# Kernel optimization log

Measured on AMD Instinct MI355X. Metric: run time of the kernel, lower is better.

The kernel has to match this reference:

```python
import jax, jax.numpy as jnp
import numpy as np


def setup_inputs() -> dict:
    N, E, F, M, D = 50000, 200000, 64, 64, 128
    L = 3
    LAMBS = jnp.array([1.0, 0.1, 0.01], jnp.float32) * 12.0  # lambs * output
    R = int(np.ceil(np.sqrt(N)))  # n_virtuals = 224
    RAW = M * L + F  # raw_message_dimension = 256
    key = jax.random.key(0)
    ks = jax.random.split(key, 16)

    def lin(k, i, o):
        return jax.random.normal(k, (i, o), jnp.float32) / np.float32(np.sqrt(i))

    return dict(
        source_nodes=jax.random.randint(ks[0], (E,), 0, N),
        target_nodes=jax.random.randint(ks[1], (E,), 0, N),
        timestamps=jax.random.uniform(ks[2], (E,), jnp.float32),
        now_time=jnp.ones((1,), jnp.float32),
        predict_IND=0,
        node_features=0.1 * jax.random.normal(ks[3], (N, F), jnp.float32),
        memory=jnp.concatenate([0.05 * jax.random.normal(ks[4], (N, L, M), jnp.float32), jnp.ones((N, L, 1), jnp.float32)], axis=-1),
        last_update=jnp.zeros((N,), jnp.float32),
        virtual_memory=0.05 * jax.random.normal(ks[5], (R, L, M), jnp.float32),
        virtual_last_update=jnp.zeros((R,), jnp.float32),
        A_r=jnp.ones((N, R), jnp.float32) + jax.random.uniform(ks[6], (N, R), jnp.float32) / 10.0,
        static_emb=0.1 * jax.random.normal(ks[7], (N, D), jnp.float32),
        lamb=jnp.array([0.5], jnp.float32),
        lambs=LAMBS,
        mf_W1=lin(ks[8], RAW, RAW // 2), mf_b1=jnp.zeros((RAW // 2,), jnp.float32),
        mf_W2=lin(ks[9], RAW // 2, M), mf_b2=jnp.zeros((M,), jnp.float32),
        ffr_W1=lin(ks[10], RAW, RAW), ffr_b1=jnp.zeros((RAW,), jnp.float32),
        ffr_W2=lin(ks[11], RAW, M), ffr_b2=jnp.zeros((M,), jnp.float32),
        et_W=lin(ks[12], L * M, M), et_b=jnp.zeros((M,), jnp.float32),
        st_W=lin(ks[13], 2 * M, D), st_b=jnp.zeros((D,), jnp.float32),
    )


def reference(source_nodes, target_nodes, timestamps, now_time, predict_IND,
              node_features, memory, last_update, virtual_memory, virtual_last_update,
              A_r, static_emb, lamb, lambs,
              mf_W1, mf_b1, mf_W2, mf_b2, ffr_W1, ffr_b1, ffr_W2, ffr_b2,
              et_W, et_b, st_W, st_b):
    N, L, Mp1 = memory.shape
    M = Mp1 - 1
    R = virtual_memory.shape[0]
    E = source_nodes.shape[0]
    eps = 1e-6

    # exp_lambs embedding of targets: memory ratio [E, L*M]
    mem_t = memory[target_nodes]
    tgt_emb = (mem_t[:, :, :-1] / mem_t[:, :, -1:]).reshape(E, L * M)
    # raw message = [target_embedding, node_features[target], 1]  -> [E, RAW+1]
    src_msg = jnp.concatenate([tgt_emb, node_features[target_nodes], jnp.ones((E, 1), tgt_emb.dtype)], axis=1)

    # exp_lambs aggregation: decay every event to the latest timestamp of its source node
    t_max = jax.ops.segment_max(timestamps, source_nodes, num_segments=N)
    cnt = jax.ops.segment_sum(jnp.ones((E,), timestamps.dtype), source_nodes, num_segments=N)
    has_msg = cnt > 0
    t_max = jnp.where(has_msg, t_max, 0.0)
    w = jnp.exp(-lambs[None, :] * (t_max[source_nodes][:, None] - timestamps[:, None]))  # [E, L]
    agg = jax.ops.segment_sum(w[:, :, None] * src_msg[:, None, :], source_nodes, num_segments=N)  # [N, L, RAW+1]

    # MLP message function on feature channels, carry the weight-count channel along
    feat = agg[:, :, :-1]  # [N, L, RAW]
    h = jax.nn.relu(feat @ mf_W1 + mf_b1)
    msg_feat = jax.nn.relu(h @ mf_W2 + mf_b2)  # [N, L, M]
    messages = jnp.concatenate([msg_feat, agg[:, :, -1:]], axis=-1)  # [N, L, M+1]

    # virtual-node routing: A = softmax(A_r, axis=0) restricted to active nodes
    A = jax.nn.softmax(A_r, axis=0) * has_msg[:, None].astype(A_r.dtype)  # [N, R]
    B = jnp.where(has_msg[:, None, None], feat / jnp.maximum(agg[:, :, -1:], eps), 0.0)  # [N, L, RAW]
    vmid = jnp.einsum('nr,nlf->rlf', A, B)  # [R, L, RAW]
    vh = jax.nn.leaky_relu(vmid @ ffr_W1 + ffr_b1)
    vmsg = jax.nn.leaky_relu(vh @ ffr_W2 + ffr_b2)  # [R, L, M]

    # node memory exp-decay update (only active nodes)
    dt = jnp.where(has_msg, t_max - last_update, 0.0)
    decay = jnp.exp(-lambs[None, :, None] * dt[:, None, None])  # [N, L, 1]
    new_mem = jnp.where(has_msg[:, None, None], memory * decay + messages, memory)
    node_emb = (new_mem[:, :, :-1] / jnp.maximum(new_mem[:, :, -1:], eps)).reshape(N, L * M)

    # virtual memory exp-decay update to now_time
    vdt = now_time[0] - virtual_last_update  # [R]
    vdecay = jnp.exp(-lambs[None, :] * vdt[:, None])  # [R, L]
    new_vmem = virtual_memory * vdecay[:, :, None] + vmsg
    v_emb = new_vmem.reshape(R, L * M)

    r2n = jax.nn.softmax(A_r, axis=1)  # [N, R]
    vnode_emb = r2n @ v_emb  # [N, L*M]

    dyn = jnp.concatenate([node_emb, vnode_emb], axis=0)  # [2N, L*M]
    hh = jax.nn.leaky_relu(dyn @ et_W + et_b)  # [2N, M]
    hh = hh.reshape(2, N, M).transpose(1, 0, 2).reshape(N, 2 * M)
    spat = jax.nn.leaky_relu(hh @ st_W + st_b)  # [N, D]
    return lamb[0] * static_emb + (1.0 - lamb[0]) * spat
```

## Files before the change

### kernel.cpp

```cpp
#include <hip/hip_runtime.h>

static __device__ __forceinline__ float lky(float x) { return x > 0.f ? x : 0.01f * x; }

static __device__ __forceinline__ unsigned short f2bf(float x) {
    unsigned int u = __float_as_uint(x);
    unsigned int r = (u + 0x7FFFu + ((u >> 16) & 1u)) >> 16;
    return (unsigned short)r;
}
static __device__ __forceinline__ float bf2f(unsigned short x) {
    return __uint_as_float((unsigned int)x << 16);
}
static __device__ __forceinline__ unsigned int pack2bf(float lo, float hi) {
    return (unsigned int)f2bf(lo) | ((unsigned int)f2bf(hi) << 16);
}

typedef __attribute__((ext_vector_type(8))) short short8;
typedef __attribute__((ext_vector_type(4))) float f32x4;

constexpr int SN  = 50048;
constexpr int KLV = 608;
constexpr int VCM = 83;
constexpr int NSCAN = 53248;

__global__ void k_init(float* t_max, int* cnt, int* cursor, float* colsum, int N, int NP) {
    int i = blockIdx.x * 256 + threadIdx.x;
    if (i < N) { t_max[i] = -1.0f; cursor[i] = 0; }
    if (i < NP) cnt[i] = 0;
    if (i < 224) colsum[i] = 0.0f;
}

__global__ void k_tbf(const float* __restrict__ src, unsigned short* __restrict__ dst,
                      int K, int C) {
    int i = blockIdx.x * 256 + threadIdx.x;
    if (i >= K * C) return;
    int c = i / K, k = i % K;
    dst[i] = f2bf(src[k * C + c]);
}

__global__ void k_tmax_cnt(const int* __restrict__ src, const float* __restrict__ ts,
                           float* t_max, int* cnt, int E) {
    int e = blockIdx.x * 256 + threadIdx.x;
    if (e >= E) return;
    int s = src[e];
    atomicMax((int*)(t_max + s), __float_as_int(ts[e]));
    atomicAdd(cnt + s, 1);
}

__global__ __launch_bounds__(1024) void k_scan(const int* __restrict__ cnt,
                                               int* __restrict__ offsets, int N) {
    __shared__ int wsum[16];
    __shared__ int s_run;
    int t = threadIdx.x;
    int lane = t & 63, wid = t >> 6;
    if (t == 0) s_run = 0;
    __syncthreads();
    int nchunk = (N + 4095) >> 12;
    for (int c = 0; c < nchunk; ++c) {
        int i0 = (c << 12) + t * 4;
        int4 v = *(const int4*)(cnt + i0);
        int s = v.x + v.y + v.z + v.w;
        int x = s;
        #pragma unroll
        for (int d = 1; d < 64; d <<= 1) {
            int y = __shfl_up(x, d, 64);
            if (lane >= d) x += y;
        }
        if (lane == 63) wsum[wid] = x;
        __syncthreads();
        int wbase = 0;
        #pragma unroll
        for (int w = 0; w < 16; ++w) wbase += (w < wid) ? wsum[w] : 0;
        int run = s_run;
        int base = run + wbase + x - s;
        if (i0 + 3 < N) {
            int4 o;
            o.x = base; o.y = base + v.x; o.z = o.y + v.y; o.w = o.z + v.z;
            *(int4*)(offsets + i0) = o;
        } else {
            int o = base;
            if (i0 < N) offsets[i0] = o;
            o += v.x;
            if (i0 + 1 < N) offsets[i0 + 1] = o;
            o += v.y;
            if (i0 + 2 < N) offsets[i0 + 2] = o;
            o += v.z;
            if (i0 + 3 < N) offsets[i0 + 3] = o;
        }
        __syncthreads();
        if (t == 1023) s_run = run + wbase + x;
        __syncthreads();
    }
    if (t == 0) offsets[N] = s_run;
}

__global__ void k_scatter(const int* __restrict__ src, const int* __restrict__ offsets,
                          int* cursor, int* sorted, int E) {
    int e = blockIdx.x * 256 + threadIdx.x;
    if (e >= E) return;
    int s = src[e];
    int pos = offsets[s] + atomicAdd(cursor + s, 1);
    sorted[pos] = e;
}

__global__ __launch_bounds__(256) void k_prep(
        const float* __restrict__ memory, const float* __restrict__ nodef,
        unsigned int* __restrict__ temb, int N) {
    int wid = threadIdx.x >> 6, lane = threadIdx.x & 63;
    int n = blockIdx.x * 4 + wid;
    if (n >= N) return;
    const float* mrow = memory + (size_t)n * 195;
    float d0 = mrow[64], d1 = mrow[129], d2 = mrow[194];
    int f = 2 * lane;
    float den = (f < 64) ? d0 : d1;
    int offA = (f < 64) ? f : f + 1;
    float va0 = mrow[offA] / den;
    float va1 = mrow[offA + 1] / den;
    float vb0, vb1;
    if (lane < 32) {
        vb0 = mrow[130 + 2 * lane] / d2;
        vb1 = mrow[131 + 2 * lane] / d2;
    } else {
        const float* nf = nodef + (size_t)n * 64 + 2 * (lane - 32);
        vb0 = nf[0]; vb1 = nf[1];
    }
    temb[(size_t)n * 128 + lane]      = pack2bf(va0, va1);
    temb[(size_t)n * 128 + 64 + lane] = pack2bf(vb0, vb1);
}

__global__ __launch_bounds__(256) void k_aexp(
        const float* __restrict__ A_r,
        float* __restrict__ rowsum, float* __restrict__ colsum,
        unsigned short* __restrict__ AexpT, unsigned short* __restrict__ Aexp_rm, int N) {
    __shared__ unsigned short sE[64][228];
    int t = threadIdx.x;
    int n0 = blockIdx.x * 64;
    int maxq = min(64, N - n0) * 56;
    const float4* src = (const float4*)(A_r + (size_t)n0 * 224);
    #pragma unroll
    for (int k = 0; k < 14; ++k) {
        int i = t + k * 256;
        float4 v = (i < maxq) ? src[i] : (float4){-1e30f, -1e30f, -1e30f, -1e30f};
        int row = i / 56, cq = i % 56;
        uint2 pk;
        pk.x = pack2bf(__expf(v.x), __expf(v.y));
        pk.y = pack2bf(__expf(v.z), __expf(v.w));
        *(uint2*)&sE[row][cq * 4] = pk;
    }
    __syncthreads();
    {
        int row = t >> 2, q = t & 3;
        const uint2* p = (const uint2*)&sE[row][q * 56];
        float s = 0.f;
        #pragma unroll
        for (int c = 0; c < 7; ++c) {
            uint2 u = p[c];
            s += __uint_as_float(u.x << 16) + __uint_as_float(u.x & 0xffff0000u)
               + __uint_as_float(u.y << 16) + __uint_as_float(u.y & 0xffff0000u);
        }
        s += __shfl_xor(s, 1, 64);
        s += __shfl_xor(s, 2, 64);
        if (q == 0 && n0 + row < N) rowsum[n0 + row] = s;
    }
    if (t < 224) {
        float s = 0.f;
        #pragma unroll 8
        for (int r = 0; r < 64; ++r) s += bf2f(sE[r][t]);
        atomicAdd(colsum + t, s);
    }
    {
        unsigned int* dst = (unsigned int*)Aexp_rm;
        for (int i = t; i < 64 * 112; i += 256) {
            int n = i / 112, cp = i % 112;
            dst[(size_t)(n0 + n) * 112 + cp] = *(const unsigned int*)&sE[n][2 * cp];
        }
    }
    {
        unsigned int* dst = (unsigned int*)AexpT;
        for (int u = t; u < 224 * 32; u += 256) {
            int r = u >> 5, np = u & 31;
            unsigned int lo = sE[2 * np][r];
            unsigned int hi = sE[2 * np + 1][r];
            dst[(size_t)r * (SN / 2) + (n0 >> 1) + np] = lo | (hi << 16);
        }
    }
}

__global__ __launch_bounds__(256) void k_agg(
        const int* __restrict__ tgt, const float* __restrict__ ts,
        const int* __restrict__ sorted, const int* __restrict__ offsets,
        const float* __restrict__ t_max, const unsigned int* __restrict__ temb,
        const float* __restrict__ lambs,
        unsigned int* __restrict__ aggb, float* __restrict__ cnt3,
        int* __restrict__ has_msg, int N) {
    int wid = threadIdx.x >> 6, lane = threadIdx.x & 63;
    int n = blockIdx.x * 4 + wid;
    size_t rb = (size_t)n * 3;
    if (n >= N) {
        #pragma unroll
        for (int l = 0; l < 3; ++l) {
            unsigned int* row = aggb + (rb + l) * 128;
            row[lane] = 0; row[64 + lane] = 0;
            if (lane == 0) cnt3[rb + l] = 0.f;
        }
        return;
    }
    int beg = offsets[n], end = offsets[n + 1];
    float lb0 = lambs[0], lb1 = lambs[1], lb2 = lambs[2];
    float tm = t_max[n];
    float aa0[3], aa1[3], ab0[3], ab1[3], accc[3];
    #pragma unroll
    for (int l = 0; l < 3; ++l) { aa0[l] = aa1[l] = ab0[l] = ab1[l] = accc[l] = 0.f; }
    for (int idx = beg; idx < end; ++idx) {
        int e = sorted[idx];
        int tt = tgt[e];
        float d = tm - ts[e];
        unsigned int ua = temb[(size_t)tt * 128 + lane];
        unsigned int ub = temb[(size_t)tt * 128 + 64 + lane];
        float a0 = __uint_as_float(ua << 16);
        float a1 = __uint_as_float(ua & 0xffff0000u);
        float b0 = __uint_as_float(ub << 16);
        float b1 = __uint_as_float(ub & 0xffff0000u);
        float w0 = __expf(-lb0 * d), w1 = __expf(-lb1 * d), w2 = __expf(-lb2 * d);
        aa0[0] += w0 * a0; aa1[0] += w0 * a1; ab0[0] += w0 * b0; ab1[0] += w0 * b1; accc[0] += w0;
        aa0[1] += w1 * a0; aa1[1] += w1 * a1; ab0[1] += w1 * b0; ab1[1] += w1 * b1; accc[1] += w1;
        aa0[2] += w2 * a0; aa1[2] += w2 * a1; ab0[2] += w2 * b0; ab1[2] += w2 * b1; accc[2] += w2;
    }
    #pragma unroll
    for (int l = 0; l < 3; ++l) {
        unsigned int* row = aggb + (rb + l) * 128;
        row[lane]      = pack2bf(aa0[l], aa1[l]);
        row[64 + lane] = pack2bf(ab0[l], ab1[l]);
        if (lane == 0) cnt3[rb + l] = accc[l];
    }
    if (lane == 0) has_msg[n] = (end > beg) ? 1 : 0;
}

__global__ __launch_bounds__(256) void k_mf_mfma(
        const unsigned short* __restrict__ aggb,
        const unsigned short* __restrict__ W1T, const float* __restrict__ b1,
        const unsigned short* __restrict__ W2T, const float* __restrict__ b2,
        unsigned short* __restrict__ msg_feat, int NROWS) {
    __shared__ unsigned short As[64 * 264];
    __shared__ unsigned short Hs[64 * 136];
    int t = threadIdx.x, lane = t & 63, w = t >> 6;
    int lr = lane & 15, kg = lane >> 4;
    int row0 = blockIdx.x * 64;
    {
        int r = t >> 2, s4 = t & 3;
        const uint4* src = (const uint4*)(aggb + (size_t)(row0 + r) * 256 + s4 * 64);
        uint4* dst = (uint4*)(As + r * 264 + s4 * 64);
        #pragma unroll
        for (int u = 0; u < 8; ++u) dst[u] = src[u];
    }
    __syncthreads();
    int n0 = w * 32;
    f32x4 acc[4][2];
    #pragma unroll
    for (int m = 0; m < 4; ++m) {
        acc[m][0] = (f32x4){0.f, 0.f, 0.f, 0.f};
        acc[m][1] = (f32x4){0.f, 0.f, 0.f, 0.f};
    }
    for (int kk = 0; kk < 8; ++kk) {
        short8 bf0 = *(const short8*)(W1T + (size_t)(n0 + lr) * 256 + kk * 32 + kg * 8);
        short8 bf1 = *(const short8*)(W1T + (size_t)(n0 + 16 + lr) * 256 + kk * 32 + kg * 8);
        #pragma unroll
        for (int m = 0; m < 4; ++m) {
            short8 af = *(const short8*)(As + (m * 16 + lr) * 264 + kk * 32 + kg * 8);
            acc[m][0] = __builtin_amdgcn_mfma_f32_16x16x32_bf16(af, bf0, acc[m][0], 0, 0, 0);
            acc[m][1] = __builtin_amdgcn_mfma_f32_16x16x32_bf16(af, bf1, acc[m][1], 0, 0, 0);
        }
    }
    float bb0 = b1[n0 + lr], bb1 = b1[n0 + 16 + lr];
    #pragma unroll
    for (int m = 0; m < 4; ++m)
        #pragma unroll
        for (int j = 0; j < 4; ++j) {
            int row = m * 16 + kg * 4 + j;
            Hs[row * 136 + n0 + lr]      = f2bf(fmaxf(acc[m][0][j] + bb0, 0.f));
            Hs[row * 136 + n0 + 16 + lr] = f2bf(fmaxf(acc[m][1][j] + bb1, 0.f));
        }
    __syncthreads();
    int c0 = w * 16;
    f32x4 a2[4];
    #pragma unroll
    for (int m = 0; m < 4; ++m) a2[m] = (f32x4){0.f, 0.f, 0.f, 0.f};
    for (int kk = 0; kk < 4; ++kk) {
        short8 bf = *(const short8*)(W2T + (size_t)(c0 + lr) * 128 + kk * 32 + kg * 8);
        #pragma unroll
        for (int m = 0; m < 4; ++m) {
            short8 af = *(const short8*)(Hs + (m * 16 + lr) * 136 + kk * 32 + kg * 8);
            a2[m] = __builtin_amdgcn_mfma_f32_16x16x32_bf16(af, bf, a2[m], 0, 0, 0);
        }
    }
    float b2v = b2[c0 + lr];
    #pragma unroll
    for (int m = 0; m < 4; ++m)
        #pragma unroll
        for (int j = 0; j < 4; ++j) {
            int row = row0 + m * 16 + kg * 4 + j;
            if (row < NROWS)
                msg_feat[(size_t)row * 64 + c0 + lr] = f2bf(fmaxf(a2[m][j] + b2v, 0.f));
        }
}

__global__ __launch_bounds__(256) void k_vmid_mfma(
        const unsigned short* __restrict__ AexpT, const unsigned short* __restrict__ aggb,
        const float* __restrict__ cnt3, float* __restrict__ vpart) {
    __shared__ unsigned short As[112 * 40];
    __shared__ unsigned int BsT[128 * 20];
    int bx = blockIdx.x;
    int chunk = bx / 12, tile = bx % 12;
    int r0 = (tile & 1) * 112;
    int ft = tile >> 1;
    int l = ft >> 1, fo = (ft & 1) * 128;
    int t = threadIdx.x, lane = t & 63, w = t >> 6;
    int lr = lane & 15, kg = lane >> 4;
    int np = t >> 4, sg = t & 15;
    f32x4 acc[7][2];
    #pragma unroll
    for (int q = 0; q < 7; ++q) {
        acc[q][0] = (f32x4){0.f, 0.f, 0.f, 0.f};
        acc[q][1] = (f32x4){0.f, 0.f, 0.f, 0.f};
    }
    int nbeg = chunk * KLV;
    int nsteps = min(KLV, SN - nbeg) >> 5;
    int c0 = w * 32 + lr, c1 = c0 + 16;
    int rb0 = c0 * 20 + (kg ^ ((c0 >> 3) & 3)) * 4;
    int rb1 = c1 * 20 + (kg ^ ((c1 >> 3) & 3)) * 4;
    int swz = np ^ ((sg & 3) << 2);
    for (int s = 0; s < nsteps; ++s) {
        int n0 = nbeg + s * 32;
        if (t < 224) {
            int srow = t >> 1, sseg = t & 1;
            const uint4* ap = (const uint4*)(AexpT + (size_t)(r0 + srow) * SN + n0) + sseg * 2;
            uint4 v0 = ap[0];
            uint4 v1 = ap[1];
            *(uint4*)&As[srow * 40 + sseg * 16]     = v0;
            *(uint4*)&As[srow * 40 + sseg * 16 + 8] = v1;
        }
        {
            int na = n0 + 2 * np;
            size_t ra = ((size_t)na * 3 + l) * 256 + fo + sg * 8;
            uint4 va = *(const uint4*)(aggb + ra);
            uint4 vb = *(const uint4*)(aggb + ra + 768);
            float da = 1.f / fmaxf(cnt3[(size_t)na * 3 + l], 1e-6f);
            float db = 1.f / fmaxf(cnt3[(size_t)na * 3 + l + 3], 1e-6f);
            const unsigned short* pa = (const unsigned short*)&va;
            const unsigned short* pb = (const unsigned short*)&vb;
            unsigned int* dst = BsT + sg * 160 + swz;
            #pragma unroll
            for (int j = 0; j < 8; ++j)
                dst[j * 20] = pack2bf(bf2f(pa[j]) * da, bf2f(pb[j]) * db);
        }
        __syncthreads();
        short8 b0 = *(const short8*)((const unsigned short*)(BsT + rb0));
        short8 b1 = *(const short8*)((const unsigned short*)(BsT + rb1));
        #pragma unroll
        for (int q = 0; q < 7; ++q) {
            short8 af = *(const short8*)&As[(q * 16 + lr) * 40 + kg * 8];
            acc[q][0] = __builtin_amdgcn_mfma_f32_16x16x32_bf16(af, b0, acc[q][0], 0, 0, 0);
            acc[q][1] = __builtin_amdgcn_mfma_f32_16x16x32_bf16(af, b1, acc[q][1], 0, 0, 0);
        }
        __syncthreads();
    }
    float* outp = vpart + (size_t)chunk * 172032;
    #pragma unroll
    for (int q = 0; q < 7; ++q) {
        int row = r0 + q * 16 + kg * 4;
        #pragma unroll
        for (int p = 0; p < 2; ++p) {
            int col = l * 256 + fo + w * 32 + p * 16 + lr;
            #pragma unroll
            for (int j = 0; j < 4; ++j)
                outp[(size_t)(row + j) * 768 + col] = acc[q][p][j];
        }
    }
}

__global__ void k_vred(const float* __restrict__ vpart, const float* __restrict__ colsum,
                       float* __restrict__ vmid) {
    int idx = blockIdx.x * 256 + threadIdx.x;
    if (idx >= 224 * 768) return;
    float s = 0.f;
    for (int c = 0; c < VCM; ++c) s += vpart[(long)c * (224 * 768) + idx];
    vmid[idx] = s / colsum[idx / 768];
}

__global__ __launch_bounds__(256) void k_ffr(
        const float* __restrict__ vmid, const float* __restrict__ W1, const float* __restrict__ b1,
        const float* __restrict__ W2, const float* __restrict__ b2,
        const float* __restrict__ vmem, const float* __restrict__ vlast,
        const float* __restrict__ lambs, const float* __restrict__ now_time,
        unsigned short* __restrict__ vembT) {
    __shared__ float sin_[16][260];
    __shared__ float svh[16][260];
    int row0 = blockIdx.x * 16;
    int t = threadIdx.x;
    #pragma unroll
    for (int k = 0; k < 16; ++k) {
        int idx = t + k * 256;
        int r = idx >> 8, f = idx & 255;
        sin_[r][f] = vmid[(long)(row0 + r) * 256 + f];
    }
    __syncthreads();
    {
        int cg = t & 63, rg = t >> 6;
        int c0 = cg * 4, r0 = rg * 4;
        float acc[4][4];
        #pragma unroll
        for (int i = 0; i < 4; ++i)
            #pragma unroll
            for (int j = 0; j < 4; ++j) acc[i][j] = 0.f;
        for (int f0 = 0; f0 < 256; f0 += 4) {
            float4 a[4];
            #pragma unroll
            for (int i = 0; i < 4; ++i) a[i] = *(const float4*)&sin_[r0 + i][f0];
            #pragma unroll
            for (int ff = 0; ff < 4; ++ff) {
                float4 w = *(const float4*)&W1[(long)(f0 + ff) * 256 + c0];
                #pragma unroll
                for (int i = 0; i < 4; ++i) {
                    float av = (&a[i].x)[ff];
                    acc[i][0] += av * w.x; acc[i][1] += av * w.y;
                    acc[i][2] += av * w.z; acc[i][3] += av * w.w;
                }
            }
        }
        #pragma unroll
        for (int i = 0; i < 4; ++i)
            #pragma unroll
            for (int j = 0; j < 4; ++j)
                svh[r0 + i][c0 + j] = lky(acc[i][j] + b1[c0 + j]);
    }
    __syncthreads();
    {
        int cg = t & 31, rg = t >> 5;
        int c0 = cg * 2, r0 = rg * 2;
        float acc[2][2];
        acc[0][0] = acc[0][1] = acc[1][0] = acc[1][1] = 0.f;
        for (int f0 = 0; f0 < 256; f0 += 4) {
            float4 a[2];
            #pragma unroll
            for (int i = 0; i < 2; ++i) a[i] = *(const float4*)&svh[r0 + i][f0];
            #pragma unroll
            for (int ff = 0; ff < 4; ++ff) {
                float2 w = *(const float2*)&W2[(long)(f0 + ff) * 64 + c0];
                #pragma unroll
                for (int i = 0; i < 2; ++i) {
                    float av = (&a[i].x)[ff];
                    acc[i][0] += av * w.x; acc[i][1] += av * w.y;
                }
            }
        }
        float nowv = now_time[0];
        #pragma unroll
        for (int i = 0; i < 2; ++i) {
            int row = row0 + r0 + i;
            int rr = row / 3, l = row % 3;
            float vd = __expf(-lambs[l] * (nowv - vlast[rr]));
            #pragma unroll
            for (int j = 0; j < 2; ++j) {
                float v = lky(acc[i][j] + b2[c0 + j]);
                int m = c0 + j;
                vembT[(size_t)(l * 64 + m) * 224 + rr] =
                    f2bf(vmem[(long)rr * 192 + l * 64 + m] * vd + v);
            }
        }
    }
}

__global__ void k_newmem(const float* __restrict__ memory,
        const unsigned short* __restrict__ msg_feat,
        const float* __restrict__ cnt3, const float* __restrict__ t_max,
        const float* __restrict__ last_update, const int* __restrict__ has_msg,
        const float* __restrict__ lambs, unsigned short* __restrict__ node_emb, int N) {
    int n = blockIdx.x;
    int j = threadIdx.x;
    int l = j >> 6, m = j & 63;
    int has = has_msg[n];
    float dt = has ? (t_max[n] - last_update[n]) : 0.f;
    float decay = __expf(-lambs[l] * dt);
    long mb = (long)n * 195 + l * 65;
    float num = memory[mb + m];
    float den = memory[mb + 64];
    if (has) {
        num = num * decay + bf2f(msg_feat[(size_t)n * 192 + j]);
        den = den * decay + cnt3[(size_t)n * 3 + l];
    }
    node_emb[(size_t)n * 192 + j] = f2bf(num / fmaxf(den, 1e-6f));
}

__global__ __launch_bounds__(256) void k_vnode_mfma(
        const unsigned short* __restrict__ Aexp_rm, const unsigned short* __restrict__ vembT,
        const float* __restrict__ rowsum, unsigned short* __restrict__ vnode_emb, int N) {
    __shared__ unsigned short As[64 * 232];
    __shared__ float sRS[64];
    int t = threadIdx.x, lane = t & 63, w = t >> 6;
    int lr = lane & 15, kg = lane >> 4;
    int row0 = blockIdx.x * 64;
    {
        int r = t >> 2, sg = t & 3;
        const uint4* src = (const uint4*)(Aexp_rm + (size_t)(row0 + r) * 224 + sg * 56);
        uint4* dst = (uint4*)(As + r * 232 + sg * 56);
        #pragma unroll
        for (int u = 0; u < 7; ++u) dst[u] = src[u];
    }
    if (t < 64) sRS[t] = rowsum[min(row0 + t, N - 1)];
    __syncthreads();
    int n0 = w * 48;
    f32x4 acc[4][3];
    #pragma unroll
    for (int m = 0; m < 4; ++m)
        #pragma unroll
        for (int nt = 0; nt < 3; ++nt) acc[m][nt] = (f32x4){0.f, 0.f, 0.f, 0.f};
    for (int kk = 0; kk < 7; ++kk) {
        short8 bf[3];
        #pragma unroll
        for (int nt = 0; nt < 3; ++nt)
            bf[nt] = *(const short8*)(vembT + (size_t)(n0 + nt * 16 + lr) * 224 + kk * 32 + kg * 8);
        #pragma unroll
        for (int m = 0; m < 4; ++m) {
            short8 af = *(const short8*)(As + (m * 16 + lr) * 232 + kk * 32 + kg * 8);
            #pragma unroll
            for (int nt = 0; nt < 3; ++nt)
                acc[m][nt] = __builtin_amdgcn_mfma_f32_16x16x32_bf16(af, bf[nt], acc[m][nt], 0, 0, 0);
        }
    }
    #pragma unroll
    for (int m = 0; m < 4; ++m)
        #pragma unroll
        for (int j = 0; j < 4; ++j) {
            int row = row0 + m * 16 + kg * 4 + j;
            if (row < N) {
                float inv = 1.f / sRS[row - row0];
                #pragma unroll
                for (int nt = 0; nt < 3; ++nt)
                    vnode_emb[(size_t)row * 192 + n0 + nt * 16 + lr] = f2bf(acc[m][nt][j] * inv);
            }
        }
}

__global__ __launch_bounds__(256) void k_et_st_mfma(
        const unsigned short* __restrict__ ne, const unsigned short* __restrict__ ve,
        const unsigned short* __restrict__ etWT, const float* __restrict__ etb,
        const unsigned short* __restrict__ stWT, const float* __restrict__ stb,
        const float* __restrict__ stat, const float* __restrict__ lamb,
        float* __restrict__ out, int N) {
    __shared__ unsigned short As[128 * 200];
    __shared__ unsigned short Hs[64 * 136];
    int t = threadIdx.x, lane = t & 63, w = t >> 6;
    int lr = lane & 15, kg = lane >> 4;
    int row0 = blockIdx.x * 64;
    {
        int r = t >> 2, sg = t & 3;
        const uint4* sn = (const uint4*)(ne + (size_t)(row0 + r) * 192 + sg * 48);
        const uint4* sv = (const uint4*)(ve + (size_t)(row0 + r) * 192 + sg * 48);
        uint4* dn = (uint4*)(As + (size_t)r * 200 + sg * 48);
        uint4* dv = (uint4*)(As + (size_t)(64 + r) * 200 + sg * 48);
        #pragma unroll
        for (int u = 0; u < 6; ++u) { dn[u] = sn[u]; dv[u] = sv[u]; }
    }
    __syncthreads();
    int c0 = w * 16;
    f32x4 acc[2][4];
    #pragma unroll
    for (int h = 0; h < 2; ++h)
        #pragma unroll
        for (int m = 0; m < 4; ++m) acc[h][m] = (f32x4){0.f, 0.f, 0.f, 0.f};
    for (int kk = 0; kk < 6; ++kk) {
        short8 bf = *(const short8*)(etWT + (size_t)(c0 + lr) * 192 + kk * 32 + kg * 8);
        #pragma unroll
        for (int h = 0; h < 2; ++h)
            #pragma unroll
            for (int m = 0; m < 4; ++m) {
                short8 af = *(const short8*)(As + (size_t)(h * 64 + m * 16 + lr) * 200 + kk * 32 + kg * 8);
                acc[h][m] = __builtin_amdgcn_mfma_f32_16x16x32_bf16(af, bf, acc[h][m], 0, 0, 0);
            }
    }
    float bb = etb[c0 + lr];
    #pragma unroll
    for (int h = 0; h < 2; ++h)
        #pragma unroll
        for (int m = 0; m < 4; ++m)
            #pragma unroll
            for (int j = 0; j < 4; ++j)
                Hs[(m * 16 + kg * 4 + j) * 136 + h * 64 + c0 + lr] = f2bf(lky(acc[h][m][j] + bb));
    __syncthreads();
    int c0s = w * 32;
    f32x4 a2[4][2];
    #pragma unroll
    for (int m = 0; m < 4; ++m) { a2[m][0] = (f32x4){0.f,0.f,0.f,0.f}; a2[m][1] = (f32x4){0.f,0.f,0.f,0.f}; }
    for (int kk = 0; kk < 4; ++kk) {
        short8 bf0 = *(const short8*)(stWT + (size_t)(c0s + lr) * 128 + kk * 32 + kg * 8);
        short8 bf1 = *(const short8*)(stWT + (size_t)(c0s + 16 + lr) * 128 + kk * 32 + kg * 8);
        #pragma unroll
        for (int m = 0; m < 4; ++m) {
            short8 af = *(const short8*)(Hs + (m * 16 + lr) * 136 + kk * 32 + kg * 8);
            a2[m][0] = __builtin_amdgcn_mfma_f32_16x16x32_bf16(af, bf0, a2[m][0], 0, 0, 0);
            a2[m][1] = __builtin_amdgcn_mfma_f32_16x16x32_bf16(af, bf1, a2[m][1], 0, 0, 0);
        }
    }
    float lam = lamb[0];
    float sb0 = stb[c0s + lr], sb1 = stb[c0s + 16 + lr];
    #pragma unroll
    for (int m = 0; m < 4; ++m)
        #pragma unroll
        for (int j = 0; j < 4; ++j) {
            int n = row0 + m * 16 + kg * 4 + j;
            if (n < N) {
                int ca = c0s + lr, cb = c0s + 16 + lr;
                float va = lky(a2[m][0][j] + sb0);
                float vb = lky(a2[m][1][j] + sb1);
                out[(size_t)n * 128 + ca] = lam * stat[(size_t)n * 128 + ca] + (1.f - lam) * va;
                out[(size_t)n * 128 + cb] = lam * stat[(size_t)n * 128 + cb] + (1.f - lam) * vb;
            }
        }
}

extern "C" void kernel_launch(void* const* d_in, const int* in_sizes, int n_in,
                              void* d_out, int out_size, void* d_ws, size_t ws_size,
                              hipStream_t stream) {
    const int*   src        = (const int*)d_in[0];
    const int*   tgt        = (const int*)d_in[1];
    const float* ts         = (const float*)d_in[2];
    const float* now_time   = (const float*)d_in[3];
    const float* nodef      = (const float*)d_in[5];
    const float* memory     = (const float*)d_in[6];
    const float* last_upd   = (const float*)d_in[7];
    const float* vmem       = (const float*)d_in[8];
    const float* vlast      = (const float*)d_in[9];
    const float* A_r        = (const float*)d_in[10];
    const float* static_emb = (const float*)d_in[11];
    const float* lamb       = (const float*)d_in[12];
    const float* lambs      = (const float*)d_in[13];
    const float* mf_W1      = (const float*)d_in[14];
    const float* mf_b1      = (const float*)d_in[15];
    const float* mf_W2      = (const float*)d_in[16];
    const float* mf_b2      = (const float*)d_in[17];
    const float* ffr_W1     = (const float*)d_in[18];
    const float* ffr_b1     = (const float*)d_in[19];
    const float* ffr_W2     = (const float*)d_in[20];
    const float* ffr_b2     = (const float*)d_in[21];
    const float* et_W       = (const float*)d_in[22];
    const float* et_b       = (const float*)d_in[23];
    const float* st_W       = (const float*)d_in[24];
    const float* st_b       = (const float*)d_in[25];

    int E = in_sizes[0];
    int N = in_sizes[7];

    float* ws = (float*)d_ws;
    size_t off = 0;
    auto alloc = [&](size_t nf) { float* p = ws + off; off += (nf + 63) & ~(size_t)63; return p; };
    unsigned short* aggb  = (unsigned short*)alloc((size_t)SN * 384);
    unsigned short* msg_feat = (unsigned short*)alloc((size_t)N * 96);
    unsigned short* AexpT   = (unsigned short*)alloc((size_t)224 * SN / 2);
    unsigned short* Aexp_rm = (unsigned short*)alloc((size_t)SN * 224 / 2);
    float* tv_union = alloc((size_t)VCM * 172032);
    float* vmid     = alloc(224 * 768);
    unsigned short* vembT = (unsigned short*)alloc((size_t)192 * 224 / 2 + 64);
    float* t_max    = alloc(N);
    float* rowsum   = alloc(N);
    float* cnt3     = alloc((size_t)SN * 3);
    float* colsum   = alloc(256);
    unsigned short* W1T  = (unsigned short*)alloc(128 * 256 / 2);
    unsigned short* W2T  = (unsigned short*)alloc(64 * 128 / 2);
    unsigned short* etWT = (unsigned short*)alloc(64 * 192 / 2);
    unsigned short* stWT = (unsigned short*)alloc(128 * 128 / 2);
    int*   cnt      = (int*)alloc(NSCAN);
    int*   offsets  = (int*)alloc(N + 1);
    int*   cursor   = (int*)alloc(N);
    int*   sorted   = (int*)alloc(E);
    int*   has_msg  = (int*)alloc(N);
    if (off * sizeof(float) > ws_size) return;

    unsigned int* temb = (unsigned int*)tv_union;
    float* vpart = tv_union;
    unsigned short* node_emb  = (unsigned short*)aggb;
    unsigned short* vnode_emb = node_emb + (size_t)N * 192;

    k_init<<<(NSCAN + 255) / 256, 256, 0, stream>>>(t_max, cnt, cursor, colsum, N, NSCAN);
    k_tbf<<<(256 * 128 + 255) / 256, 256, 0, stream>>>(mf_W1, W1T, 256, 128);
    k_tbf<<<(128 * 64 + 255) / 256, 256, 0, stream>>>(mf_W2, W2T, 128, 64);
    k_tbf<<<(192 * 64 + 255) / 256, 256, 0, stream>>>(et_W, etWT, 192, 64);
    k_tbf<<<(128 * 128 + 255) / 256, 256, 0, stream>>>(st_W, stWT, 128, 128);
    k_tmax_cnt<<<(E + 255) / 256, 256, 0, stream>>>(src, ts, t_max, cnt, E);
    k_scan<<<1, 1024, 0, stream>>>(cnt, offsets, N);
    k_scatter<<<(E + 255) / 256, 256, 0, stream>>>(src, offsets, cursor, sorted, E);
    k_prep<<<(N + 3) / 4, 256, 0, stream>>>(memory, nodef, temb, N);
    k_aexp<<<SN / 64, 256, 0, stream>>>(A_r, rowsum, colsum, AexpT, Aexp_rm, N);
    k_agg<<<SN / 4, 256, 0, stream>>>(tgt, ts, sorted, offsets, t_max, temb,
                                      lambs, (unsigned int*)aggb, cnt3, has_msg, N);
    k_mf_mfma<<<SN * 3 / 64, 256, 0, stream>>>(aggb, W1T, mf_b1, W2T, mf_b2, msg_feat, N * 3);
    k_vmid_mfma<<<12 * VCM, 256, 0, stream>>>(AexpT, aggb, cnt3, vpart);
    k_vred<<<(224 * 768 + 255) / 256, 256, 0, stream>>>(vpart, colsum, vmid);
    k_ffr<<<42, 256, 0, stream>>>(vmid, ffr_W1, ffr_b1, ffr_W2, ffr_b2, vmem, vlast,
                                  lambs, now_time, vembT);
    k_newmem<<<N, 192, 0, stream>>>(memory, msg_feat, cnt3, t_max, last_upd, has_msg,
                                    lambs, node_emb, N);
    k_vnode_mfma<<<SN / 64, 256, 0, stream>>>(Aexp_rm, vembT, rowsum, vnode_emb, N);
    k_et_st_mfma<<<SN / 64, 256, 0, stream>>>(node_emb, vnode_emb, etWT, et_b, stWT, st_b,
                                              static_emb, lamb, (float*)d_out, N);
}
```

Before: 385.0 us.

## Read MFMA A-operands directly from global and remap vmid blocks per XCD

Three MFMA kernels (mf, vnode, et_st) no longer stage their A tiles in shared memory. Each wave now loads its A fragments straight from global memory, which removes the LDS copy and a barrier and lowers LDS use so more blocks can be resident. The cost is that every wave re-reads the same A rows from global/L2 instead of sharing one LDS copy. Separately, the vmid kernel remaps block IDs so that consecutive virtual blocks, which share chunks of the A and aggregate data, land on the same XCD for better L2 locality.

```diff
diff --git a/kernel.cpp b/kernel.cpp
--- a/kernel.cpp
+++ b/kernel.cpp
@@ -21,6 +21,9 @@
 constexpr int KLV = 608;
 constexpr int VCM = 83;
 constexpr int NSCAN = 53248;
+constexpr int NWG_V = 12 * VCM;
+constexpr int NQ_V  = NWG_V / 8;
+constexpr int NR_V  = NWG_V % 8;
 
 __global__ void k_init(float* t_max, int* cnt, int* cursor, float* colsum, int N, int NP) {
     int i = blockIdx.x * 256 + threadIdx.x;
@@ -240,19 +243,11 @@
         const unsigned short* __restrict__ W1T, const float* __restrict__ b1,
         const unsigned short* __restrict__ W2T, const float* __restrict__ b2,
         unsigned short* __restrict__ msg_feat, int NROWS) {
-    __shared__ unsigned short As[64 * 264];
     __shared__ unsigned short Hs[64 * 136];
     int t = threadIdx.x, lane = t & 63, w = t >> 6;
     int lr = lane & 15, kg = lane >> 4;
     int row0 = blockIdx.x * 64;
-    {
-        int r = t >> 2, s4 = t & 3;
-        const uint4* src = (const uint4*)(aggb + (size_t)(row0 + r) * 256 + s4 * 64);
-        uint4* dst = (uint4*)(As + r * 264 + s4 * 64);
-        #pragma unroll
-        for (int u = 0; u < 8; ++u) dst[u] = src[u];
-    }
-    __syncthreads();
+    const unsigned short* abase = aggb + (size_t)row0 * 256;
     int n0 = w * 32;
     f32x4 acc[4][2];
     #pragma unroll
@@ -265,7 +260,7 @@
         short8 bf1 = *(const short8*)(W1T + (size_t)(n0 + 16 + lr) * 256 + kk * 32 + kg * 8);
         #pragma unroll
         for (int m = 0; m < 4; ++m) {
-            short8 af = *(const short8*)(As + (m * 16 + lr) * 264 + kk * 32 + kg * 8);
+            short8 af = *(const short8*)(abase + (size_t)(m * 16 + lr) * 256 + kk * 32 + kg * 8);
             acc[m][0] = __builtin_amdgcn_mfma_f32_16x16x32_bf16(af, bf0, acc[m][0], 0, 0, 0);
             acc[m][1] = __builtin_amdgcn_mfma_f32_16x16x32_bf16(af, bf1, acc[m][1], 0, 0, 0);
         }
@@ -309,7 +304,10 @@
     __shared__ unsigned short As[112 * 40];
     __shared__ unsigned int BsT[128 * 20];
     int bx = blockIdx.x;
-    int chunk = bx / 12, tile = bx % 12;
+    int xcd = bx & 7, bidx = bx >> 3;
+    int virt = (xcd < NR_V) ? xcd * (NQ_V + 1) + bidx
+                            : NR_V * (NQ_V + 1) + (xcd - NR_V) * NQ_V + bidx;
+    int chunk = virt / 12, tile = virt % 12;
     int r0 = (tile & 1) * 112;
     int ft = tile >> 1;
     int l = ft >> 1, fo = (ft & 1) * 128;
@@ -493,18 +491,11 @@
 __global__ __launch_bounds__(256) void k_vnode_mfma(
         const unsigned short* __restrict__ Aexp_rm, const unsigned short* __restrict__ vembT,
         const float* __restrict__ rowsum, unsigned short* __restrict__ vnode_emb, int N) {
-    __shared__ unsigned short As[64 * 232];
     __shared__ float sRS[64];
     int t = threadIdx.x, lane = t & 63, w = t >> 6;
     int lr = lane & 15, kg = lane >> 4;
     int row0 = blockIdx.x * 64;
-    {
-        int r = t >> 2, sg = t & 3;
-        const uint4* src = (const uint4*)(Aexp_rm + (size_t)(row0 + r) * 224 + sg * 56);
-        uint4* dst = (uint4*)(As + r * 232 + sg * 56);
-        #pragma unroll
-        for (int u = 0; u < 7; ++u) dst[u] = src[u];
-    }
+    const unsigned short* abase = Aexp_rm + (size_t)row0 * 224;
     if (t < 64) sRS[t] = rowsum[min(row0 + t, N - 1)];
     __syncthreads();
     int n0 = w * 48;
@@ -520,7 +511,7 @@
             bf[nt] = *(const short8*)(vembT + (size_t)(n0 + nt * 16 + lr) * 224 + kk * 32 + kg * 8);
         #pragma unroll
         for (int m = 0; m < 4; ++m) {
-            short8 af = *(const short8*)(As + (m * 16 + lr) * 232 + kk * 32 + kg * 8);
+            short8 af = *(const short8*)(abase + (size_t)(m * 16 + lr) * 224 + kk * 32 + kg * 8);
             #pragma unroll
             for (int nt = 0; nt < 3; ++nt)
                 acc[m][nt] = __builtin_amdgcn_mfma_f32_16x16x32_bf16(af, bf[nt], acc[m][nt], 0, 0, 0);
@@ -546,21 +537,10 @@
         const unsigned short* __restrict__ stWT, const float* __restrict__ stb,
         const float* __restrict__ stat, const float* __restrict__ lamb,
         float* __restrict__ out, int N) {
-    __shared__ unsigned short As[128 * 200];
     __shared__ unsigned short Hs[64 * 136];
     int t = threadIdx.x, lane = t & 63, w = t >> 6;
     int lr = lane & 15, kg = lane >> 4;
     int row0 = blockIdx.x * 64;
-    {
-        int r = t >> 2, sg = t & 3;
-        const uint4* sn = (const uint4*)(ne + (size_t)(row0 + r) * 192 + sg * 48);
-        const uint4* sv = (const uint4*)(ve + (size_t)(row0 + r) * 192 + sg * 48);
-        uint4* dn = (uint4*)(As + (size_t)r * 200 + sg * 48);
-        uint4* dv = (uint4*)(As + (size_t)(64 + r) * 200 + sg * 48);
-        #pragma unroll
-        for (int u = 0; u < 6; ++u) { dn[u] = sn[u]; dv[u] = sv[u]; }
-    }
-    __syncthreads();
     int c0 = w * 16;
     f32x4 acc[2][4];
     #pragma unroll
@@ -570,12 +550,14 @@
     for (int kk = 0; kk < 6; ++kk) {
         short8 bf = *(const short8*)(etWT + (size_t)(c0 + lr) * 192 + kk * 32 + kg * 8);
         #pragma unroll
-        for (int h = 0; h < 2; ++h)
+        for (int h = 0; h < 2; ++h) {
+            const unsigned short* abase = (h == 0) ? ne : ve;
             #pragma unroll
             for (int m = 0; m < 4; ++m) {
-                short8 af = *(const short8*)(As + (size_t)(h * 64 + m * 16 + lr) * 200 + kk * 32 + kg * 8);
+                short8 af = *(const short8*)(abase + (size_t)(row0 + m * 16 + lr) * 192 + kk * 32 + kg * 8);
                 acc[h][m] = __builtin_amdgcn_mfma_f32_16x16x32_bf16(af, bf, acc[h][m], 0, 0, 0);
             }
+        }
     }
     float bb = etb[c0 + lr];
     #pragma unroll
@@ -692,7 +674,7 @@
     k_agg<<<SN / 4, 256, 0, stream>>>(tgt, ts, sorted, offsets, t_max, temb,
                                       lambs, (unsigned int*)aggb, cnt3, has_msg, N);
     k_mf_mfma<<<SN * 3 / 64, 256, 0, stream>>>(aggb, W1T, mf_b1, W2T, mf_b2, msg_feat, N * 3);
-    k_vmid_mfma<<<12 * VCM, 256, 0, stream>>>(AexpT, aggb, cnt3, vpart);
+    k_vmid_mfma<<<NWG_V, 256, 0, stream>>>(AexpT, aggb, cnt3, vpart);
     k_vred<<<(224 * 768 + 255) / 256, 256, 0, stream>>>(vpart, colsum, vmid);
     k_ffr<<<42, 256, 0, stream>>>(vmid, ffr_W1, ffr_b1, ffr_W2, ffr_b2, vmem, vlast,
                                   lambs, now_time, vembT);
```

Measured after the change: 409.0 us. 6.2% more time.
